# Performance work log

Measured on AMD Instinct MI355X. Metric: run time of the kernel, lower is better.

## Reference

```python
import jax, jax.numpy as jnp
import numpy as np


def _resize_bilinear(x, h, w):
    # matches F.upsample(mode='bilinear', align_corners=False) (half-pixel centers)
    return jax.image.resize(x, (x.shape[0], x.shape[1], h, w), method='bilinear')


def _build_volume_2d(fl, fr, maxdisp):
    # fl, fr: [B,C,H,W] -> cost [B,D,H,W], D=maxdisp (stride=1)
    B, C, H, W = fl.shape
    d = jnp.arange(maxdisp)
    src = jnp.arange(W)[None, :] - d[:, None]          # [D,W]
    valid = (src >= 0).astype(fl.dtype)
    src_c = jnp.clip(src, 0, W - 1)
    fr_sh = fr[:, :, :, src_c] * valid                  # [B,C,H,D,W]; zeros where w<d
    cost = jnp.abs(fl[:, :, :, None, :] - fr_sh).sum(axis=1)  # [B,H,D,W]
    return jnp.transpose(cost, (0, 2, 1, 3))            # [B,D,H,W]


def _warp(fr, disp):
    # fr: [B,C,H,W]; disp: [B,K,H,W] horizontal disparity (sample at x - disp)
    # bilinear along W, zero padding (grid_sample semantics, align_corners=True grid)
    B, C, H, W = fr.shape
    xs = jnp.arange(W, dtype=fr.dtype)[None, None, None, :] - disp   # [B,K,H,W]
    x0 = jnp.floor(xs)
    w1 = xs - x0                                        # frac weight for right neighbor
    x0i = x0.astype(jnp.int32)
    x1i = x0i + 1
    v0 = ((x0i >= 0) & (x0i < W)).astype(fr.dtype)
    v1 = ((x1i >= 0) & (x1i < W)).astype(fr.dtype)
    x0c = jnp.clip(x0i, 0, W - 1)
    x1c = jnp.clip(x1i, 0, W - 1)

    def gather(idx):  # idx [B,K,H,W] -> [B,K,C,H,W]
        idxb = jnp.broadcast_to(idx[:, :, None, :, :], (B, idx.shape[1], C, H, W))
        return jnp.take_along_axis(fr[:, None], idxb, axis=-1)

    g0 = gather(x0c) * v0[:, :, None]
    g1 = gather(x1c) * v1[:, :, None]
    return g0 * (1.0 - w1)[:, :, None] + g1 * w1[:, :, None]   # [B,K,C,H,W]


def _build_volume_2d3(fl, fr, maxdisp, disp):
    # fl, fr: [B,C,H,W]; disp: [B,1,H,W] coarse disparity. K = 2*maxdisp-1 shifts.
    shifts = jnp.arange(-maxdisp + 1, maxdisp, dtype=fl.dtype)       # [K]
    bd = disp - shifts[None, :, None, None]                          # [B,K,H,W]
    warped = _warp(fr, bd)                                           # [B,K,C,H,W]
    return jnp.abs(fl[:, None] - warped).sum(axis=2)                 # [B,K,H,W]


def _regress(cost, start, end):
    # softmax(-cost) over disparity axis, weighted sum with disp values [start,end)
    p = jax.nn.softmax(-cost, axis=1)
    dvals = jnp.arange(start, end, dtype=cost.dtype)[None, :, None, None]
    return jnp.sum(p * dvals, axis=1, keepdims=True)                 # [B,1,H,W]


def setup_inputs() -> dict:
    key = jax.random.key(0)
    k = jax.random.split(key, 4)
    return {
        "feat_l0": jax.random.normal(k[0], (4, 32, 64, 128), dtype=jnp.float32),
        "feat_r0": jax.random.normal(k[1], (4, 32, 64, 128), dtype=jnp.float32),
        "feat_l1": jax.random.normal(k[2], (4, 32, 128, 256), dtype=jnp.float32),
        "feat_r1": jax.random.normal(k[3], (4, 32, 128, 256), dtype=jnp.float32),
        "img_h": 512,
        "img_w": 1024,
        "maxdisp0": 12,
        "maxdisp1": 3,
    }


def reference(feat_l0, feat_r0, feat_l1, feat_r1, img_h, img_w, maxdisp0, maxdisp1):
    H0 = feat_l0.shape[2]
    H1, W1 = feat_l1.shape[2], feat_l1.shape[3]

    cost0 = _build_volume_2d(feat_l0, feat_r0, maxdisp0)             # [B,D0,H0,W0]
    pred_low0 = _regress(cost0, 0, maxdisp0) * (img_h / H0)
    pred0 = _resize_bilinear(pred_low0, img_h, img_w)                # [B,1,img_h,img_w]

    # ---- scale 1: residual cost volume via warp around coarse disparity ----
    wflow = _resize_bilinear(pred0, H1, W1) * (H1 / img_h)           # [B,1,H1,W1]
    cost1 = _build_volume_2d3(feat_l1, feat_r1, maxdisp1, wflow)     # [B,2*D1-1,H1,W1]
    pred_low1 = _regress(cost1, -maxdisp1 + 1, maxdisp1) * (img_h / H1)
    pred1 = _resize_bilinear(pred_low1, img_h, img_w) + pred0

    return (pred0, pred1)
```

## Files before the change

kernel.cpp:

```cpp
#include <hip/hip_runtime.h>

#define NB 4
#define NC 32
#define H0 64
#define W0 128
#define D0 12
#define H1 128
#define W1 256
#define NK 5
#define IMH 512
#define IMW 1024

#define FR0_STRIDE 52
#define FR0_GUARD  16
#define FR1_STRIDE 164
#define FR1_GUARD  28

__global__ __launch_bounds__(256, 4) void k_cost0(const float* __restrict__ fl,
                                                  const float* __restrict__ fr,
                                                  float* __restrict__ pl0) {
    const int blk = blockIdx.x;
    const int row = blk >> 2;
    const int quarter = blk & 3;
    const int w0 = quarter * 32;
    const int b = row >> 6, h = row & (H0 - 1);
    const int tid = threadIdx.x;
    __shared__ float frs[NC][FR0_STRIDE];

    const size_t rowbase = ((size_t)b * NC * H0 + h) * W0;

    const int wloc = tid >> 3, g = tid & 7;

    float flv[4];
#pragma unroll
    for (int j = 0; j < 4; ++j)
        flv[j] = fl[rowbase + (size_t)(g + 8 * j) * (H0 * W0) + w0 + wloc];

#pragma unroll
    for (int i = 0; i < 2; ++i) {
        int idx = i * 256 + tid;
        if (idx < NC * 12) {
            int c = idx / 12, q = idx - c * 12;
            int colg = w0 - 16 + q * 4;
            float4 v = make_float4(0.f, 0.f, 0.f, 0.f);
            if (colg >= 0)
                v = *(const float4*)(fr + rowbase + (size_t)c * (H0 * W0) + colg);
            *(float4*)&frs[c][q * 4] = v;
        }
    }
    __syncthreads();

    float cost[D0];
#pragma unroll
    for (int d = 0; d < D0; ++d) cost[d] = 0.f;
#pragma unroll
    for (int j = 0; j < 4; ++j) {
        int c = g + 8 * j;
        const float* sr = &frs[c][FR0_GUARD + wloc];
#pragma unroll
        for (int d = 0; d < D0; ++d)
            cost[d] += fabsf(flv[j] - sr[-d]);
    }
#pragma unroll
    for (int d = 0; d < D0; ++d) {
        cost[d] += __shfl_xor(cost[d], 1);
        cost[d] += __shfl_xor(cost[d], 2);
        cost[d] += __shfl_xor(cost[d], 4);
    }
    if (g == 0) {
        float m = cost[0];
#pragma unroll
        for (int d = 1; d < D0; ++d) m = fminf(m, cost[d]);
        float s = 0.f, sd = 0.f;
#pragma unroll
        for (int d = 0; d < D0; ++d) {
            float e = expf(m - cost[d]);
            s += e;
            sd += (float)d * e;
        }
        pl0[(size_t)row * W0 + w0 + wloc] = 8.f * (sd / s);
    }
}

__global__ __launch_bounds__(256, 4) void k_cost1(const float* __restrict__ fl,
                                                  const float* __restrict__ fr,
                                                  const float* __restrict__ pl0,
                                                  float* __restrict__ pl1) {
    const int blk = blockIdx.x;
    const int half = blk & 1;
    const int w0 = half * 128;
    const int rowid = blk >> 1;
    const int b = rowid >> 7, oy = rowid & (H1 - 1);
    const int tid = threadIdx.x;
    __shared__ float frs1[NC][FR1_STRIDE];
    __shared__ float ytmp[W0];
    __shared__ float wfl[W1];

    const size_t rowbase1 = ((size_t)b * NC * H1 + oy) * W1;

#pragma unroll
    for (int i = 0; i < 5; ++i) {
        int idx = i * 256 + tid;
        int c = idx / 40, q = idx - c * 40;
        int colg = w0 - FR1_GUARD + q * 4;
        float4 v = make_float4(0.f, 0.f, 0.f, 0.f);
        if (colg >= 0 && colg <= W1 - 4)
            v = *(const float4*)(fr + rowbase1 + (size_t)c * (H1 * W1) + colg);
        *(float4*)&frs1[c][q * 4] = v;
    }

    const int w = w0 + (tid >> 1), hh = tid & 1;
    float flv[16];
#pragma unroll
    for (int j = 0; j < 16; ++j)
        flv[j] = fl[rowbase1 + (size_t)(2 * j + hh) * (H1 * W1) + w];

    if (tid < W0) {
        const float* p0b = pl0 + (size_t)b * H0 * W0;
        int m = oy >> 1;
        int r0, r1, r2;
        float wy0, wy1, wy2;
        if (oy == 0) {
            r0 = 0; r1 = 0; r2 = 1;
            wy0 = 0.f; wy1 = 27.625f / 28.f; wy2 = 0.375f / 28.f;
        } else if (oy == H1 - 1) {
            r0 = H0 - 2; r1 = H0 - 1; r2 = H0 - 1;
            wy0 = 0.375f / 28.f; wy1 = 27.625f / 28.f; wy2 = 0.f;
        } else {
            r0 = max(m - 1, 0); r1 = m; r2 = min(m + 1, H0 - 1);
            if (oy & 1) { wy0 = 0.375f / 32.f; wy1 = 23.25f / 32.f; wy2 = 8.375f / 32.f; }
            else        { wy0 = 8.375f / 32.f; wy1 = 23.25f / 32.f; wy2 = 0.375f / 32.f; }
        }
        ytmp[tid] = wy0 * p0b[r0 * W0 + tid] + wy1 * p0b[r1 * W0 + tid]
                  + wy2 * p0b[r2 * W0 + tid];
    }
    __syncthreads();

    {
        int ox = tid, n = ox >> 1;
        int c0, c1, c2;
        float wx0, wx1, wx2;
        if (ox == 0) {
            c0 = 0; c1 = 0; c2 = 1;
            wx0 = 0.f; wx1 = 27.625f / 28.f; wx2 = 0.375f / 28.f;
        } else if (ox == W1 - 1) {
            c0 = W0 - 2; c1 = W0 - 1; c2 = W0 - 1;
            wx0 = 0.375f / 28.f; wx1 = 27.625f / 28.f; wx2 = 0.f;
        } else {
            c0 = max(n - 1, 0); c1 = n; c2 = min(n + 1, W0 - 1);
            if (ox & 1) { wx0 = 0.375f / 32.f; wx1 = 23.25f / 32.f; wx2 = 8.375f / 32.f; }
            else        { wx0 = 8.375f / 32.f; wx1 = 23.25f / 32.f; wx2 = 0.375f / 32.f; }
        }
        wfl[ox] = 0.25f * (wx0 * ytmp[c0] + wx1 * ytmp[c1] + wx2 * ytmp[c2]);
    }
    __syncthreads();

    {
        float disp = wfl[w];
        float xs = (float)w - disp;
        float xbf = floorf(xs);
        float f = xs - xbf;
        int xb = (int)xbf;
        const float* sr = &frs1[0][FR1_GUARD + (xb - w0) - 2];

        float cost[NK];
#pragma unroll
        for (int k = 0; k < NK; ++k) cost[k] = 0.f;
#pragma unroll
        for (int j = 0; j < 16; ++j) {
            int c = 2 * j + hh;
            const float* row = sr + c * FR1_STRIDE;
            float g0 = row[0], g1 = row[1], g2 = row[2];
            float g3 = row[3], g4 = row[4], g5 = row[5];
            float flvj = flv[j];
            cost[0] += fabsf(flvj - (g0 + f * (g1 - g0)));
            cost[1] += fabsf(flvj - (g1 + f * (g2 - g1)));
            cost[2] += fabsf(flvj - (g2 + f * (g3 - g2)));
            cost[3] += fabsf(flvj - (g3 + f * (g4 - g3)));
            cost[4] += fabsf(flvj - (g5 * f + g4 * (1.f - f)));
        }
#pragma unroll
        for (int k = 0; k < NK; ++k) cost[k] += __shfl_xor(cost[k], 1);
        if (hh == 0) {
            float m = cost[0];
#pragma unroll
            for (int k = 1; k < NK; ++k) m = fminf(m, cost[k]);
            float s = 0.f, sd = 0.f;
#pragma unroll
            for (int k = 0; k < NK; ++k) {
                float e = expf(m - cost[k]);
                s += e;
                sd += (float)(k - 2) * e;
            }
            pl1[(size_t)rowid * W1 + w] = 4.f * (sd / s);
        }
    }
}

__global__ __launch_bounds__(256, 4) void k_final(const float* __restrict__ pl0,
                                                  const float* __restrict__ pl1,
                                                  float* __restrict__ out) {
    const int blk = blockIdx.x;
    const int b = blk >> 9, y = blk & (IMH - 1);
    const int tid = threadIdx.x;
    __shared__ float a0[W0];
    __shared__ float a1[W1];

    const float* p0b = pl0 + (size_t)b * H0 * W0;
    const float* p1b = pl1 + (size_t)b * H1 * W1;

    float sy0 = (y + 0.5f) * 0.125f - 0.5f;
    float y0f = floorf(sy0);
    float fy0 = sy0 - y0f;
    int r0 = (int)y0f;
    int r0c = min(max(r0, 0), H0 - 1), r1c = min(max(r0 + 1, 0), H0 - 1);

    float sy1 = (y + 0.5f) * 0.25f - 0.5f;
    float y1f = floorf(sy1);
    float fy1 = sy1 - y1f;
    int s0 = (int)y1f;
    int s0c = min(max(s0, 0), H1 - 1), s1c = min(max(s0 + 1, 0), H1 - 1);

    if (tid < W0) {
        float u = p0b[r0c * W0 + tid], v = p0b[r1c * W0 + tid];
        a0[tid] = u + fy0 * (v - u);
    }
    {
        float u = p1b[s0c * W1 + tid], v = p1b[s1c * W1 + tid];
        a1[tid] = u + fy1 * (v - u);
    }
    __syncthreads();

    float v0[4], v1[4];
#pragma unroll
    for (int i = 0; i < 4; ++i) {
        int x = tid * 4 + i;
        float sx0 = (x + 0.5f) * 0.125f - 0.5f;
        float x0f = floorf(sx0);
        float fx0 = sx0 - x0f;
        int c0 = (int)x0f;
        int c0c = min(max(c0, 0), W0 - 1), c1c = min(max(c0 + 1, 0), W0 - 1);
        float p0 = a0[c0c] + fx0 * (a0[c1c] - a0[c0c]);

        float sx1 = (x + 0.5f) * 0.25f - 0.5f;
        float x1f = floorf(sx1);
        float fx1 = sx1 - x1f;
        int d0 = (int)x1f;
        int d0c = min(max(d0, 0), W1 - 1), d1c = min(max(d0 + 1, 0), W1 - 1);
        float p1 = a1[d0c] + fx1 * (a1[d1c] - a1[d0c]);

        v0[i] = p0;
        v1[i] = p1 + p0;
    }
    const size_t NPXQ = (size_t)NB * IMH * IMW / 4;
    size_t t = (size_t)blk * 256 + tid;
    ((float4*)out)[t] = make_float4(v0[0], v0[1], v0[2], v0[3]);
    ((float4*)out)[NPXQ + t] = make_float4(v1[0], v1[1], v1[2], v1[3]);
}

extern "C" void kernel_launch(void* const* d_in, const int* in_sizes, int n_in,
                              void* d_out, int out_size, void* d_ws, size_t ws_size,
                              hipStream_t stream) {
    const float* fl0 = (const float*)d_in[0];
    const float* fr0 = (const float*)d_in[1];
    const float* fl1 = (const float*)d_in[2];
    const float* fr1 = (const float*)d_in[3];
    float* out = (float*)d_out;

    float* ws = (float*)d_ws;
    float* pl0 = ws;
    float* pl1 = ws + 32768;

    k_cost0<<<NB * H0 * 4, 256, 0, stream>>>(fl0, fr0, pl0);
    k_cost1<<<NB * H1 * 2, 256, 0, stream>>>(fl1, fr1, pl0, pl1);
    k_final<<<NB * IMH, 256, 0, stream>>>(pl0, pl1, out);
}
```

Before: 26.94 us.

## Process full rows per block in cost kernels to remove halo reloads

```diff
diff --git a/kernel.cpp b/kernel.cpp
--- a/kernel.cpp
+++ b/kernel.cpp
@@ -11,42 +11,37 @@
 #define IMH 512
 #define IMW 1024
 
-#define FR0_STRIDE 52
-#define FR0_GUARD  16
-#define FR1_STRIDE 164
-#define FR1_GUARD  28
-
-__global__ __launch_bounds__(256, 4) void k_cost0(const float* __restrict__ fl,
-                                                  const float* __restrict__ fr,
-                                                  float* __restrict__ pl0) {
+#define S0 144
+#define G0 16
+#define S1 288
+#define G1 28
+
+__global__ __launch_bounds__(256) void k_cost0(const float* __restrict__ fl,
+                                               const float* __restrict__ fr,
+                                               float* __restrict__ pl0) {
     const int blk = blockIdx.x;
-    const int row = blk >> 2;
-    const int quarter = blk & 3;
-    const int w0 = quarter * 32;
-    const int b = row >> 6, h = row & (H0 - 1);
+    const int b = blk >> 6, h = blk & (H0 - 1);
     const int tid = threadIdx.x;
-    __shared__ float frs[NC][FR0_STRIDE];
+    const int w = tid >> 1, half = tid & 1;
+    __shared__ float frs[NC][S0];
 
     const size_t rowbase = ((size_t)b * NC * H0 + h) * W0;
 
-    const int wloc = tid >> 3, g = tid & 7;
-
-    float flv[4];
-#pragma unroll
-    for (int j = 0; j < 4; ++j)
-        flv[j] = fl[rowbase + (size_t)(g + 8 * j) * (H0 * W0) + w0 + wloc];
-
-#pragma unroll
-    for (int i = 0; i < 2; ++i) {
+    float flv[16];
+#pragma unroll
+    for (int j = 0; j < 16; ++j)
+        flv[j] = fl[rowbase + (size_t)(16 * half + j) * (H0 * W0) + w];
+
+#pragma unroll
+    for (int i = 0; i < 4; ++i) {
         int idx = i * 256 + tid;
-        if (idx < NC * 12) {
-            int c = idx / 12, q = idx - c * 12;
-            int colg = w0 - 16 + q * 4;
-            float4 v = make_float4(0.f, 0.f, 0.f, 0.f);
-            if (colg >= 0)
-                v = *(const float4*)(fr + rowbase + (size_t)c * (H0 * W0) + colg);
-            *(float4*)&frs[c][q * 4] = v;
-        }
+        int c = idx >> 5, q = idx & 31;
+        *(float4*)&frs[c][G0 + q * 4] =
+            *(const float4*)(fr + rowbase + (size_t)c * (H0 * W0) + q * 4);
+    }
+    if (tid < 128) {
+        int c = tid >> 2, u = tid & 3;
+        *(float4*)&frs[c][u * 4] = make_float4(0.f, 0.f, 0.f, 0.f);
     }
     __syncthreads();
 
@@ -54,66 +49,62 @@
 #pragma unroll
     for (int d = 0; d < D0; ++d) cost[d] = 0.f;
 #pragma unroll
-    for (int j = 0; j < 4; ++j) {
-        int c = g + 8 * j;
-        const float* sr = &frs[c][FR0_GUARD + wloc];
+    for (int j = 0; j < 16; ++j) {
+        const float* sr = &frs[16 * half + j][G0 + w];
+        float fv = flv[j];
 #pragma unroll
         for (int d = 0; d < D0; ++d)
-            cost[d] += fabsf(flv[j] - sr[-d]);
-    }
-#pragma unroll
-    for (int d = 0; d < D0; ++d) {
+            cost[d] += fabsf(fv - sr[-d]);
+    }
+#pragma unroll
+    for (int d = 0; d < D0; ++d)
         cost[d] += __shfl_xor(cost[d], 1);
-        cost[d] += __shfl_xor(cost[d], 2);
-        cost[d] += __shfl_xor(cost[d], 4);
-    }
-    if (g == 0) {
-        float m = cost[0];
-#pragma unroll
-        for (int d = 1; d < D0; ++d) m = fminf(m, cost[d]);
+
+    if (half == 0) {
+        float mn = cost[0];
+#pragma unroll
+        for (int d = 1; d < D0; ++d) mn = fminf(mn, cost[d]);
         float s = 0.f, sd = 0.f;
 #pragma unroll
         for (int d = 0; d < D0; ++d) {
-            float e = expf(m - cost[d]);
+            float e = expf(mn - cost[d]);
             s += e;
             sd += (float)d * e;
         }
-        pl0[(size_t)row * W0 + w0 + wloc] = 8.f * (sd / s);
-    }
-}
-
-__global__ __launch_bounds__(256, 4) void k_cost1(const float* __restrict__ fl,
-                                                  const float* __restrict__ fr,
-                                                  const float* __restrict__ pl0,
-                                                  float* __restrict__ pl1) {
+        pl0[(size_t)blk * W0 + w] = 8.f * (sd / s);
+    }
+}
+
+__global__ __launch_bounds__(256) void k_cost1(const float* __restrict__ fl,
+                                               const float* __restrict__ fr,
+                                               const float* __restrict__ pl0,
+                                               float* __restrict__ pl1) {
     const int blk = blockIdx.x;
-    const int half = blk & 1;
-    const int w0 = half * 128;
-    const int rowid = blk >> 1;
-    const int b = rowid >> 7, oy = rowid & (H1 - 1);
+    const int b = blk >> 7, oy = blk & (H1 - 1);
     const int tid = threadIdx.x;
-    __shared__ float frs1[NC][FR1_STRIDE];
+    __shared__ float frs1[NC][S1];
     __shared__ float ytmp[W0];
     __shared__ float wfl[W1];
 
     const size_t rowbase1 = ((size_t)b * NC * H1 + oy) * W1;
 
-#pragma unroll
-    for (int i = 0; i < 5; ++i) {
+    float flv[32];
+#pragma unroll
+    for (int c = 0; c < NC; ++c)
+        flv[c] = fl[rowbase1 + (size_t)c * (H1 * W1) + tid];
+
+#pragma unroll
+    for (int i = 0; i < 8; ++i) {
         int idx = i * 256 + tid;
-        int c = idx / 40, q = idx - c * 40;
-        int colg = w0 - FR1_GUARD + q * 4;
-        float4 v = make_float4(0.f, 0.f, 0.f, 0.f);
-        if (colg >= 0 && colg <= W1 - 4)
-            v = *(const float4*)(fr + rowbase1 + (size_t)c * (H1 * W1) + colg);
-        *(float4*)&frs1[c][q * 4] = v;
-    }
-
-    const int w = w0 + (tid >> 1), hh = tid & 1;
-    float flv[16];
-#pragma unroll
-    for (int j = 0; j < 16; ++j)
-        flv[j] = fl[rowbase1 + (size_t)(2 * j + hh) * (H1 * W1) + w];
+        int c = idx >> 6, q = idx & 63;
+        *(float4*)&frs1[c][G1 + q * 4] =
+            *(const float4*)(fr + rowbase1 + (size_t)c * (H1 * W1) + q * 4);
+    }
+    {
+        int c = tid >> 3, u = tid & 7;
+        int col = (u < 7) ? u * 4 : (G1 + W1);
+        *(float4*)&frs1[c][col] = make_float4(0.f, 0.f, 0.f, 0.f);
+    }
 
     if (tid < W0) {
         const float* p0b = pl0 + (size_t)b * H0 * W0;
@@ -156,44 +147,39 @@
     __syncthreads();
 
     {
-        float disp = wfl[w];
-        float xs = (float)w - disp;
+        float disp = wfl[tid];
+        float xs = (float)tid - disp;
         float xbf = floorf(xs);
         float f = xs - xbf;
         int xb = (int)xbf;
-        const float* sr = &frs1[0][FR1_GUARD + (xb - w0) - 2];
+        const float* sr = &frs1[0][G1 + xb - 2];
 
         float cost[NK];
 #pragma unroll
         for (int k = 0; k < NK; ++k) cost[k] = 0.f;
 #pragma unroll
-        for (int j = 0; j < 16; ++j) {
-            int c = 2 * j + hh;
-            const float* row = sr + c * FR1_STRIDE;
+        for (int c = 0; c < NC; ++c) {
+            const float* row = sr + c * S1;
             float g0 = row[0], g1 = row[1], g2 = row[2];
             float g3 = row[3], g4 = row[4], g5 = row[5];
-            float flvj = flv[j];
-            cost[0] += fabsf(flvj - (g0 + f * (g1 - g0)));
-            cost[1] += fabsf(flvj - (g1 + f * (g2 - g1)));
-            cost[2] += fabsf(flvj - (g2 + f * (g3 - g2)));
-            cost[3] += fabsf(flvj - (g3 + f * (g4 - g3)));
-            cost[4] += fabsf(flvj - (g5 * f + g4 * (1.f - f)));
-        }
-#pragma unroll
-        for (int k = 0; k < NK; ++k) cost[k] += __shfl_xor(cost[k], 1);
-        if (hh == 0) {
-            float m = cost[0];
-#pragma unroll
-            for (int k = 1; k < NK; ++k) m = fminf(m, cost[k]);
-            float s = 0.f, sd = 0.f;
-#pragma unroll
-            for (int k = 0; k < NK; ++k) {
-                float e = expf(m - cost[k]);
-                s += e;
-                sd += (float)(k - 2) * e;
-            }
-            pl1[(size_t)rowid * W1 + w] = 4.f * (sd / s);
-        }
+            float fv = flv[c];
+            cost[0] += fabsf(fv - (g0 + f * (g1 - g0)));
+            cost[1] += fabsf(fv - (g1 + f * (g2 - g1)));
+            cost[2] += fabsf(fv - (g2 + f * (g3 - g2)));
+            cost[3] += fabsf(fv - (g3 + f * (g4 - g3)));
+            cost[4] += fabsf(fv - (g5 * f + g4 * (1.f - f)));
+        }
+        float mn = cost[0];
+#pragma unroll
+        for (int k = 1; k < NK; ++k) mn = fminf(mn, cost[k]);
+        float s = 0.f, sd = 0.f;
+#pragma unroll
+        for (int k = 0; k < NK; ++k) {
+            float e = expf(mn - cost[k]);
+            s += e;
+            sd += (float)(k - 2) * e;
+        }
+        pl1[(size_t)blk * W1 + tid] = 4.f * (sd / s);
     }
 }
 
@@ -271,7 +257,7 @@
     float* pl0 = ws;
     float* pl1 = ws + 32768;
 
-    k_cost0<<<NB * H0 * 4, 256, 0, stream>>>(fl0, fr0, pl0);
-    k_cost1<<<NB * H1 * 2, 256, 0, stream>>>(fl1, fr1, pl0, pl1);
+    k_cost0<<<NB * H0, 256, 0, stream>>>(fl0, fr0, pl0);
+    k_cost1<<<NB * H1, 256, 0, stream>>>(fl1, fr1, pl0, pl1);
     k_final<<<NB * IMH, 256, 0, stream>>>(pl0, pl1, out);
 }
```

Result: faster. 26.39 us (-2.0%).
